# Performance work log

Hardware: AMD Instinct MI355X
Metric: run time of the kernel (lower is better)

## Reference

```python
import jax, jax.numpy as jnp
import numpy as np

B, L, D, RATIO = 256, 197, 768, 8
DK = D // RATIO  # 96


def _mk_linear(key, out_f, in_f):
    kw, kb = jax.random.split(key)
    W = jax.random.normal(kw, (out_f, in_f), jnp.float32) * 0.02  # xavier_normal gain=0.02 scale
    b = jax.random.normal(kb, (out_f,), jnp.float32) * 0.02
    return W, b


def setup_inputs() -> dict:
    key = jax.random.key(0)
    ks = jax.random.split(key, 10)
    x = jax.random.normal(ks[0], (B, L, D), jnp.float32)
    y = jax.random.normal(ks[1], (B, L, D), jnp.float32)
    Wk1, bk1 = _mk_linear(ks[2], DK, D)
    Wk2, bk2 = _mk_linear(ks[3], DK, D)
    Wks, bks = _mk_linear(ks[4], DK, DK)
    Wl1, bl1 = _mk_linear(ks[5], L, L)
    Wl2, bl2 = _mk_linear(ks[6], L, L)
    Wv1, bv1 = _mk_linear(ks[7], D, D)
    Wv2, bv2 = _mk_linear(ks[8], D, D)
    # torch inits gammas to 0; use small nonzero values so outputs/grads are non-trivial
    g = jax.random.normal(ks[9], (2,), jnp.float32) * 0.1
    gamma1 = g[:1]
    gamma2 = g[1:]
    return dict(x=x, y=y, Wk1=Wk1, bk1=bk1, Wk2=Wk2, bk2=bk2, Wks=Wks, bks=bks,
                Wl1=Wl1, bl1=bl1, Wl2=Wl2, bl2=bl2, Wv1=Wv1, bv1=bv1,
                Wv2=Wv2, bv2=bv2, gamma1=gamma1, gamma2=gamma2)


def reference(x, y, Wk1, bk1, Wk2, bk2, Wks, bks, Wl1, bl1, Wl2, bl2,
              Wv1, bv1, Wv2, bv2, gamma1, gamma2):
    b, l, d = x.shape
    # shared-projected keys (B, L, DK)
    k1 = (x @ Wk1.T + bk1) @ Wks.T + bks
    k2 = (y @ Wk2.T + bk2) @ Wks.T + bks
    # faithful to torch: .view(B, -1, L) is a raw reshape (scrambles layout), then permute
    k1r = k1.reshape(b, -1, l).swapaxes(1, 2)   # (B, L, DK)
    k2r = k2.reshape(b, -1, l)                  # (B, DK, L)
    energy = jnp.einsum('blc,bcm->blm', k1r, k2r)  # (B, L, L)
    att1 = jax.nn.softmax(energy @ Wl1.T + bl1, axis=-1)                   # att_y_on_x
    att2 = jax.nn.softmax(energy.swapaxes(1, 2) @ Wl2.T + bl2, axis=-1)    # att_x_on_y
    v2 = y @ Wv2.T + bv2  # (B, L, D)
    out_y_on_x = jnp.einsum('bdl,blm->bdm', v2.swapaxes(1, 2), att1).reshape(b, l, d)
    out_x = gamma1 * out_y_on_x + x
    v1 = x @ Wv1.T + bv1
    out_x_on_y = jnp.einsum('bdl,blm->bdm', v1.swapaxes(1, 2), att2).reshape(b, l, d)
    out_y = gamma2 * out_x_on_y + y
    return (out_x, out_y)
```

## Files before the change

### kernel.cpp

```cpp
#include <hip/hip_runtime.h>
#include <math.h>

typedef unsigned short ushort;
typedef __attribute__((ext_vector_type(8))) short short8;
typedef __attribute__((ext_vector_type(8))) unsigned short ushort8;
typedef __attribute__((ext_vector_type(4))) float f32x4;
typedef unsigned int u32;

#define VM_WAIT(N) asm volatile("s_waitcnt vmcnt(" #N ")" ::: "memory")
#define SBAR() asm volatile("s_barrier" ::: "memory")

__device__ __forceinline__ int swz4(int row) {
  return (row & 3) ^ ((row >> 2) & 3);
}

__device__ __forceinline__ ushort f2bf(float f) {
  u32 u = __float_as_uint(f);
  return (ushort)((u + 0x7FFF + ((u >> 16) & 1)) >> 16);
}
__device__ __forceinline__ float bf2f(ushort u) {
  u32 v = ((u32)u) << 16;
  return __uint_as_float(v);
}

__device__ __forceinline__ void gload16(const void* g, void* l) {
  __builtin_amdgcn_global_load_lds(
      (const __attribute__((address_space(1))) u32*)g,
      (__attribute__((address_space(3))) u32*)l, 16, 0, 0);
}

#define BKK 32
#define LDSP 68
__global__ __launch_bounds__(256) void gemm_generic(
    const float* __restrict__ A, const float* __restrict__ Bm, const float* __restrict__ Bm2,
    float* __restrict__ C, float* __restrict__ C2,
    int M, int N, int K, long sAi, long sAk, long sBj, long sBk, long sCi)
{
  __shared__ __align__(16) float lds_a[BKK * LDSP];
  __shared__ __align__(16) float lds_b[BKK * LDSP];
  const float* Bb = blockIdx.z ? Bm2 : Bm;
  float* Cc = blockIdx.z ? C2 : C;
  const int i0 = blockIdx.y * 64;
  const int j0 = blockIdx.x * 64;
  const int tid = threadIdx.x;
  const int tx = tid & 15, ty = tid >> 4;
  float acc[4][4] = {};
  for (int k0 = 0; k0 < K; k0 += BKK) {
    for (int idx = tid; idx < BKK * 64; idx += 256) {
      int kk = idx & (BKK - 1), ii = idx >> 5;
      int gi = i0 + ii, gk = k0 + kk;
      lds_a[kk * LDSP + ii] = (gi < M && gk < K) ? A[(long)gi * sAi + (long)gk * sAk] : 0.f;
    }
    for (int idx = tid; idx < BKK * 64; idx += 256) {
      int kk = idx & (BKK - 1), jj = idx >> 5;
      int gj = j0 + jj, gk = k0 + kk;
      lds_b[kk * LDSP + jj] = (gj < N && gk < K) ? Bb[(long)gj * sBj + (long)gk * sBk] : 0.f;
    }
    __syncthreads();
    #pragma unroll
    for (int kk = 0; kk < BKK; ++kk) {
      const float4 a4 = *reinterpret_cast<const float4*>(&lds_a[kk * LDSP + ty * 4]);
      const float4 b4 = *reinterpret_cast<const float4*>(&lds_b[kk * LDSP + tx * 4]);
      const float av[4] = {a4.x, a4.y, a4.z, a4.w};
      const float bv[4] = {b4.x, b4.y, b4.z, b4.w};
      #pragma unroll
      for (int a = 0; a < 4; ++a)
        #pragma unroll
        for (int b = 0; b < 4; ++b)
          acc[a][b] = fmaf(av[a], bv[b], acc[a][b]);
    }
    __syncthreads();
  }
  for (int a = 0; a < 4; ++a) {
    int gi = i0 + ty * 4 + a;
    if (gi >= M) continue;
    for (int b = 0; b < 4; ++b) {
      int gj = j0 + tx * 4 + b;
      if (gj >= N) continue;
      Cc[(long)gi * sCi + gj] = acc[a][b];
    }
  }
}

__global__ __launch_bounds__(256) void mfma_gemm(
    const ushort* __restrict__ A0, const ushort* __restrict__ A1,
    const ushort* __restrict__ B0, const ushort* __restrict__ B1,
    const float* __restrict__ bias0, const float* __restrict__ bias1,
    float* __restrict__ C0, float* __restrict__ C1,
    int M, int N, int K, long sAi, long sBj, long sCi)
{
  __shared__ ushort As[128 * 64];
  __shared__ ushort Bs[128 * 64];
  const int which = blockIdx.z;
  const ushort* Ab = which ? A1 : A0;
  const ushort* Bb = which ? B1 : B0;
  const float* bias = which ? bias1 : bias0;
  float* C = which ? C1 : C0;
  const int i0 = blockIdx.y * 128;
  const int j0 = blockIdx.x * 128;
  const int tid = threadIdx.x;
  const int wave = tid >> 6, lane = tid & 63;
  const int wm = wave >> 1, wn = wave & 1;
  const int col16 = lane & 15, krow = lane >> 4;

  f32x4 acc[4][4] = {};

  for (int k0 = 0; k0 < K; k0 += 64) {
    #pragma unroll
    for (int it = 0; it < 4; ++it) {
      int chunk = it * 256 + wave * 64 + lane;
      int row = chunk >> 3, s = chunk & 7;
      int kc = s ^ (row & 7);
      int gi = i0 + row; if (gi >= M) gi = M - 1;
      gload16(Ab + (long)gi * sAi + k0 + kc * 8, &As[chunk * 8]);
    }
    #pragma unroll
    for (int it = 0; it < 4; ++it) {
      int chunk = it * 256 + wave * 64 + lane;
      int row = chunk >> 3, s = chunk & 7;
      int kc = s ^ (row & 7);
      int gj = j0 + row; if (gj >= N) gj = N - 1;
      gload16(Bb + (long)gj * sBj + k0 + kc * 8, &Bs[chunk * 8]);
    }
    __syncthreads();
    #pragma unroll
    for (int ks = 0; ks < 2; ++ks) {
      short8 af[4], bfr[4];
      #pragma unroll
      for (int mi = 0; mi < 4; ++mi) {
        int row = wm * 64 + mi * 16 + col16;
        int slot = (ks * 4 + krow) ^ (row & 7);
        af[mi] = *(const short8*)&As[row * 64 + slot * 8];
      }
      #pragma unroll
      for (int nj = 0; nj < 4; ++nj) {
        int row = wn * 64 + nj * 16 + col16;
        int slot = (ks * 4 + krow) ^ (row & 7);
        bfr[nj] = *(const short8*)&Bs[row * 64 + slot * 8];
      }
      #pragma unroll
      for (int mi = 0; mi < 4; ++mi)
        #pragma unroll
        for (int nj = 0; nj < 4; ++nj)
          acc[mi][nj] = __builtin_amdgcn_mfma_f32_16x16x32_bf16(
              af[mi], bfr[nj], acc[mi][nj], 0, 0, 0);
    }
    __syncthreads();
  }

  const int r0 = krow * 4;
  #pragma unroll
  for (int mi = 0; mi < 4; ++mi) {
    int gi0 = i0 + wm * 64 + mi * 16 + r0;
    #pragma unroll
    for (int nj = 0; nj < 4; ++nj) {
      int gj = j0 + wn * 64 + nj * 16 + col16;
      f32x4 a = acc[mi][nj];
      #pragma unroll
      for (int r = 0; r < 4; ++r) {
        int gi = gi0 + r;
        if (gi >= M || gj >= N) continue;
        C[(long)gi * sCi + gj] = a[r] + bias[gj];
      }
    }
  }
}

__global__ __launch_bounds__(256) void att_gemm(
    const ushort* __restrict__ Wl0, const ushort* __restrict__ Wl1,
    const ushort* __restrict__ E0, const ushort* __restrict__ E1,
    const float* __restrict__ bl0, const float* __restrict__ bl1,
    ushort* __restrict__ a0, ushort* __restrict__ a1out)
{
  __shared__ ushort Aws[2][208 * 32];
  __shared__ ushort Bws[2][64 * 32];
  __shared__ float blds[208];
  const int which = blockIdx.z;
  const int bz = blockIdx.y;
  const ushort* Wl = which ? Wl1 : Wl0;
  const ushort* Bb = (which ? E1 : E0) + 50432L * bz;
  const float* bl = which ? bl1 : bl0;
  ushort* aout = which ? a1out : a0;
  const int l0 = blockIdx.x * 64;
  const int tid = threadIdx.x, wave = tid >> 6, lane = tid & 63;
  const int col16 = lane & 15, kq = lane >> 4;

  if (tid < 208) blds[tid] = (tid < 197) ? bl[tid] : 0.f;

  f32x4 acc[13] = {};

  auto stage = [&](int buf, int k0) {
    const int lrow = lane >> 2, s = lane & 3;
    #pragma unroll
    for (int c0 = 0; c0 < 5; ++c0) {
      int c = wave + c0 * 4;
      if (c >= 17) break;
      if (c < 13) {
        int row = c * 16 + lrow;
        int gr = row < 197 ? row : 196;
        int kc = s ^ swz4(row);
        gload16(Wl + (long)gr * 256 + k0 + kc * 8,
                (char*)(&Aws[buf][0]) + c * 1024 + lane * 16);
      } else {
        int row = (c - 13) * 16 + lrow;
        int gl = l0 + row; if (gl > 196) gl = 196;
        int kc = s ^ swz4(row);
        gload16(Bb + (long)gl * 256 + k0 + kc * 8,
                (char*)(&Bws[buf][0]) + (c - 13) * 1024 + lane * 16);
      }
    }
  };

  stage(0, 0);
  for (int t = 0; t < 7; ++t) {
    int cur = t & 1;
    if (t + 1 < 7) {
      stage(cur ^ 1, (t + 1) * 32);
      if (wave == 0) VM_WAIT(5); else VM_WAIT(4);
    } else {
      VM_WAIT(0);
    }
    SBAR();
    int brow = wave * 16 + col16;
    short8 bf = *(const short8*)((const char*)(&Bws[cur][0]) +
                                 brow * 64 + ((kq ^ swz4(brow)) << 4));
    #pragma unroll
    for (int j = 0; j < 13; ++j) {
      int arow = j * 16 + col16;
      short8 af = *(const short8*)((const char*)(&Aws[cur][0]) +
                                   arow * 64 + ((kq ^ swz4(arow)) << 4));
      acc[j] = __builtin_amdgcn_mfma_f32_16x16x32_bf16(af, bf, acc[j], 0, 0, 0);
    }
    SBAR();
  }

  const int c = l0 + wave * 16 + col16;
  float mx = -INFINITY;
  #pragma unroll
  for (int j = 0; j < 13; ++j)
    #pragma unroll
    for (int r = 0; r < 4; ++r) {
      int m = j * 16 + kq * 4 + r;
      float v = acc[j][r] + blds[m];
      v = (m < 197) ? v : -INFINITY;
      acc[j][r] = v;
      mx = fmaxf(mx, v);
    }
  mx = fmaxf(mx, __shfl_xor(mx, 16));
  mx = fmaxf(mx, __shfl_xor(mx, 32));
  float s = 0.f;
  #pragma unroll
  for (int j = 0; j < 13; ++j)
    #pragma unroll
    for (int r = 0; r < 4; ++r) {
      int m = j * 16 + kq * 4 + r;
      float e = (m < 197) ? __expf(acc[j][r] - mx) : 0.f;
      acc[j][r] = e;
      s += e;
    }
  s += __shfl_xor(s, 16);
  s += __shfl_xor(s, 32);
  const float inv = 1.f / s;
  ushort* ab = aout + 50432L * bz;
  #pragma unroll
  for (int j = 0; j < 13; ++j)
    #pragma unroll
    for (int r = 0; r < 4; ++r) {
      int m = j * 16 + kq * 4 + r;
      if (m < 197)
        ab[(long)m * 256 + c] = (c < 197) ? f2bf(acc[j][r] * inv) : (ushort)0;
    }
}

__global__ __launch_bounds__(256) void vout_gemm(
    const ushort* __restrict__ A0, const ushort* __restrict__ A1,
    const ushort* __restrict__ B0, const ushort* __restrict__ B1,
    const float* __restrict__ bias0, const float* __restrict__ bias1,
    const ushort* __restrict__ resid0, const ushort* __restrict__ resid1,
    const float* __restrict__ g0, const float* __restrict__ g1,
    void* __restrict__ C0, void* __restrict__ C1,
    int N, int K, long sAi, long bAs, long sBj, long bBs,
    long sCi, long bCs, int mtiles, int batches, int mode)
{
  __shared__ ushort As[2][128 * 32];
  __shared__ ushort Bs[2][224 * 32];
  const int per = mtiles * batches;
  int bid = blockIdx.x;
  const int which = bid / per;
  bid -= which * per;
  const ushort* A = which ? A1 : A0;
  const ushort* Bm = which ? B1 : B0;
  const float* bias = which ? bias1 : bias0;
  const ushort* resid = which ? resid1 : resid0;
  const float* gammaPtr = which ? g1 : g0;
  void* C = which ? C1 : C0;

  int mtile, bz;
  if ((batches & 7) == 0) {
    int xcd = bid & 7, sid = bid >> 3;
    mtile = sid % mtiles;
    bz = (sid / mtiles) * 8 + xcd;
  } else {
    mtile = bid % mtiles;
    bz = bid / mtiles;
  }
  const ushort* Ab = A + bAs * bz + (long)(mtile * 128) * sAi;
  const ushort* Bb = Bm + bBs * bz;
  const int tid = threadIdx.x, wave = tid >> 6, lane = tid & 63;
  const int wr = wave >> 1, wc = wave & 1;
  const int col16 = lane & 15, kq = lane >> 4;

  f32x4 acc[4][7] = {};

  auto stage = [&](int buf, int k0) {
    const int lrow = lane >> 2, s = lane & 3;
    #pragma unroll
    for (int c0 = 0; c0 < 6; ++c0) {
      int c = wave + c0 * 4;
      if (c >= 22) break;
      if (c < 8) {
        int row = c * 16 + lrow;
        int kc = s ^ swz4(row);
        gload16(Ab + (long)row * sAi + k0 + kc * 8,
                (char*)(&As[buf][0]) + c * 1024 + lane * 16);
      } else {
        int row = (c - 8) * 16 + lrow;
        int gj = row < N ? row : N - 1;
        int kc = s ^ swz4(row);
        gload16(Bb + (long)gj * sBj + k0 + kc * 8,
                (char*)(&Bs[buf][0]) + (c - 8) * 1024 + lane * 16);
      }
    }
  };

  const int nt = K >> 5;
  stage(0, 0);
  for (int t = 0; t < nt; ++t) {
    int cur = t & 1;
    if (t + 1 < nt) {
      stage(cur ^ 1, (t + 1) << 5);
      if (wave < 2) VM_WAIT(6); else VM_WAIT(5);
    } else {
      VM_WAIT(0);
    }
    SBAR();
    short8 af[4];
    #pragma unroll
    for (int mi = 0; mi < 4; ++mi) {
      int arow = wr * 64 + mi * 16 + col16;
      af[mi] = *(const short8*)((const char*)(&As[cur][0]) +
                                arow * 64 + ((kq ^ swz4(arow)) << 4));
    }
    #pragma unroll
    for (int nj = 0; nj < 7; ++nj) {
      int brow = wc * 112 + nj * 16 + col16;
      short8 bf = *(const short8*)((const char*)(&Bs[cur][0]) +
                                   brow * 64 + ((kq ^ swz4(brow)) << 4));
      #pragma unroll
      for (int mi = 0; mi < 4; ++mi)
        acc[mi][nj] = __builtin_amdgcn_mfma_f32_16x16x32_bf16(
            af[mi], bf, acc[mi][nj], 0, 0, 0);
    }
    SBAR();
  }

  if (mode == 3) {
    const float g = gammaPtr[0];
    #pragma unroll
    for (int mi = 0; mi < 4; ++mi)
      #pragma unroll
      for (int nj = 0; nj < 7; ++nj) {
        int gj = wc * 112 + nj * 16 + col16;
        if (gj >= N) continue;
        #pragma unroll
        for (int r = 0; r < 4; ++r) {
          int gi = mtile * 128 + wr * 64 + mi * 16 + kq * 4 + r;
          long ci = bCs * bz + (long)gi * sCi + gj;
          ((float*)C)[ci] = g * acc[mi][nj][r] + bf2f(resid[ci]);
        }
      }
  } else {
    #pragma unroll
    for (int mi = 0; mi < 4; ++mi)
      #pragma unroll
      for (int r = 0; r < 4; ++r) {
        int gi = mtile * 128 + wr * 64 + mi * 16 + kq * 4 + r;
        long base = bCs * bz + (long)gi * sCi;
        #pragma unroll
        for (int nj = 0; nj < 7; ++nj) {
          int gj = wc * 112 + nj * 16 + col16;
          ((ushort*)C)[base + gj] = (gj < N) ? f2bf(acc[mi][nj][r] + bias[gi])
                                             : (ushort)0;
        }
      }
  }
}

__global__ __launch_bounds__(256) void energy_dual(
    const float* __restrict__ k1, const float* __restrict__ k2,
    ushort* __restrict__ Eb, ushort* __restrict__ ETb)
{
  __shared__ __align__(16) float lds[2][BKK * LDSP];
  const int bz = blockIdx.z;
  const float* Ab = k1 + 18912L * bz;
  const float* Bb = k2 + 18912L * bz;
  const int i0 = blockIdx.y * 64;
  const int j0 = blockIdx.x * 64;
  const int tid = threadIdx.x;
  const int tx = tid & 15, ty = tid >> 4;
  float acc[4][4] = {};
  for (int k0 = 0; k0 < 96; k0 += BKK) {
    for (int idx = tid; idx < BKK * 64; idx += 256) {
      int ii = idx & 63, kk = idx >> 6;
      int gi = i0 + ii, gk = k0 + kk;
      lds[0][kk * LDSP + ii] = (gi < 197 && gk < 96) ? Ab[(long)gk * 197 + gi] : 0.f;
    }
    for (int idx = tid; idx < BKK * 64; idx += 256) {
      int jj = idx & 63, kk = idx >> 6;
      int gj = j0 + jj, gk = k0 + kk;
      lds[1][kk * LDSP + jj] = (gj < 197 && gk < 96) ? Bb[(long)gk * 197 + gj] : 0.f;
    }
    __syncthreads();
    #pragma unroll
    for (int kk = 0; kk < BKK; ++kk) {
      const float4 a4 = *reinterpret_cast<const float4*>(&lds[0][kk * LDSP + ty * 4]);
      const float4 b4 = *reinterpret_cast<const float4*>(&lds[1][kk * LDSP + tx * 4]);
      const float av[4] = {a4.x, a4.y, a4.z, a4.w};
      const float bv[4] = {b4.x, b4.y, b4.z, b4.w};
      #pragma unroll
      for (int a = 0; a < 4; ++a)
        #pragma unroll
        for (int b = 0; b < 4; ++b)
          acc[a][b] = fmaf(av[a], bv[b], acc[a][b]);
    }
    __syncthreads();
  }
  float* trans = &lds[0][0];
  #pragma unroll
  for (int a = 0; a < 4; ++a)
    #pragma unroll
    for (int b = 0; b < 4; ++b)
      trans[(ty * 4 + a) * 68 + tx * 4 + b] = acc[a][b];
  __syncthreads();
  #pragma unroll
  for (int a2 = 0; a2 < 4; ++a2) {
    int lrow = ty * 4 + a2;
    int gl = i0 + lrow;
    if (gl < 197) {
      #pragma unroll
      for (int b2 = 0; b2 < 4; ++b2) {
        int gm = j0 + tx + 16 * b2;
        float v = trans[lrow * 68 + tx + 16 * b2];
        Eb[bz * 50432L + (long)gl * 256 + gm] = (gm < 197) ? f2bf(v) : (ushort)0;
      }
    }
  }
  #pragma unroll
  for (int a2 = 0; a2 < 4; ++a2) {
    int mrow = ty * 4 + a2;
    int gm = j0 + mrow;
    if (gm < 197) {
      #pragma unroll
      for (int b2 = 0; b2 < 4; ++b2) {
        int gl = i0 + tx + 16 * b2;
        float v = trans[(tx + 16 * b2) * 68 + mrow];
        ETb[bz * 50432L + (long)gm * 256 + gl] = (gl < 197) ? f2bf(v) : (ushort)0;
      }
    }
  }
}

__global__ void fuse_bias2(const float* __restrict__ Wks,
                           const float* __restrict__ bk1, const float* __restrict__ bk2,
                           const float* __restrict__ bks,
                           float* __restrict__ bf1, float* __restrict__ bf2) {
  int c = threadIdx.x;
  if (c >= 192) return;
  const float* bk = (c < 96) ? bk1 : bk2;
  float* bf = (c < 96) ? bf1 : bf2;
  int cc = (c < 96) ? c : c - 96;
  float s = bks[cc];
  for (int e = 0; e < 96; ++e) s += Wks[cc * 96 + e] * bk[e];
  bf[cc] = s;
}

__global__ __launch_bounds__(256) void conv_weights(
    const float* __restrict__ Wf1, const float* __restrict__ Wf2,
    const float* __restrict__ Wv1, const float* __restrict__ Wv2,
    const float* __restrict__ Wl1, const float* __restrict__ Wl2,
    ushort* __restrict__ Wf1b, ushort* __restrict__ Wf2b,
    ushort* __restrict__ Wv1b, ushort* __restrict__ Wv2b,
    ushort* __restrict__ Wl1b, ushort* __restrict__ Wl2b)
{
  const long total = 147456 + 1179648 + 100864;
  long stride = (long)gridDim.x * blockDim.x;
  for (long i = (long)blockIdx.x * blockDim.x + threadIdx.x; i < total; i += stride) {
    if (i < 147456) {
      long j = i;
      if (j < 73728) Wf1b[j] = f2bf(Wf1[j]);
      else Wf2b[j - 73728] = f2bf(Wf2[j - 73728]);
    } else if (i < 147456 + 1179648) {
      long j = i - 147456;
      if (j < 589824) Wv1b[j] = f2bf(Wv1[j]);
      else Wv2b[j - 589824] = f2bf(Wv2[j - 589824]);
    } else {
      long j = i - 147456 - 1179648;
      int w2 = j >= 50432;
      if (w2) j -= 50432;
      int r = (int)(j >> 8), cc = (int)(j & 255);
      const float* s = w2 ? Wl2 : Wl1;
      ushort* d = w2 ? Wl2b : Wl1b;
      d[j] = (cc < 197) ? f2bf(s[(long)r * 197 + cc]) : (ushort)0;
    }
  }
}

__global__ __launch_bounds__(256) void conv_xy(const float* __restrict__ x,
                                               const float* __restrict__ y,
                                               ushort* __restrict__ xb,
                                               ushort* __restrict__ yb, long n8) {
  long i = (long)blockIdx.x * blockDim.x + threadIdx.x;
  long stride = (long)gridDim.x * blockDim.x;
  for (; i < 2 * n8; i += stride) {
    const float* s = (i < n8) ? x : y;
    ushort* d = (i < n8) ? xb : yb;
    long j = (i < n8) ? i : i - n8;
    float4 a = ((const float4*)s)[2 * j];
    float4 b = ((const float4*)s)[2 * j + 1];
    ushort8 o;
    o[0] = f2bf(a.x); o[1] = f2bf(a.y); o[2] = f2bf(a.z); o[3] = f2bf(a.w);
    o[4] = f2bf(b.x); o[5] = f2bf(b.y); o[6] = f2bf(b.z); o[7] = f2bf(b.w);
    *(ushort8*)&d[j * 8] = o;
  }
}

extern "C" void kernel_launch(void* const* d_in, const int* in_sizes, int n_in,
                              void* d_out, int out_size, void* d_ws, size_t ws_size,
                              hipStream_t stream) {
  const float* x   = (const float*)d_in[0];
  const float* y   = (const float*)d_in[1];
  const float* Wk1 = (const float*)d_in[2];
  const float* bk1 = (const float*)d_in[3];
  const float* Wk2 = (const float*)d_in[4];
  const float* bk2 = (const float*)d_in[5];
  const float* Wks = (const float*)d_in[6];
  const float* bks = (const float*)d_in[7];
  const float* Wl1 = (const float*)d_in[8];
  const float* bl1 = (const float*)d_in[9];
  const float* Wl2 = (const float*)d_in[10];
  const float* bl2 = (const float*)d_in[11];
  const float* Wv1 = (const float*)d_in[12];
  const float* bv1 = (const float*)d_in[13];
  const float* Wv2 = (const float*)d_in[14];
  const float* bv2 = (const float*)d_in[15];
  const float* gamma1 = (const float*)d_in[16];
  const float* gamma2 = (const float*)d_in[17];
  float* out = (float*)d_out;

  const int B = 256, L = 197, D = 768;
  const long LD  = (long)L * D;
  const long LDK = (long)L * 96;

  const size_t staticBytes = 3446784;
  const size_t perB = 605184 + 151296 + 201728 + 201728 + 786432;
  int Bc = 256;
  while (Bc > 8 && staticBytes + (size_t)Bc * perB > ws_size) Bc >>= 1;

  char* p = (char*)d_ws;
  auto carve = [&](size_t bytes) { char* r = p; p += bytes; return r; };
  float*  Wf1   = (float*)carve(73728 * 4);
  float*  Wf2   = (float*)carve(73728 * 4);
  float*  bf1   = (float*)carve(512);
  float*  bf2   = (float*)carve(512);
  ushort* Wv1b  = (ushort*)carve(589824 * 2);
  ushort* Wv2b  = (ushort*)carve(589824 * 2);
  ushort* Wf1b  = (ushort*)carve(73728 * 2);
  ushort* Wf2b  = (ushort*)carve(73728 * 2);
  ushort* Wl1b  = (ushort*)carve(50432 * 2);
  ushort* Wl2b  = (ushort*)carve(50432 * 2);
  ushort* xb    = (ushort*)carve((size_t)Bc * LD * 2);
  ushort* yb    = (ushort*)carve((size_t)Bc * LD * 2);
  float*  k1    = (float*)carve((size_t)Bc * LDK * 4);
  float*  k2    = (float*)carve((size_t)Bc * LDK * 4);
  ushort* Eb    = (ushort*)carve((size_t)Bc * 50432 * 2);
  ushort* ETbuf = (ushort*)carve((size_t)Bc * 50432 * 2);
  ushort* a1    = (ushort*)carve((size_t)Bc * 50432 * 2);
  ushort* a2    = (ushort*)carve((size_t)Bc * 50432 * 2);
  ushort* vT    = (ushort*)carve((size_t)Bc * 196608 * 2);
  ushort* vT2   = (ushort*)carve((size_t)Bc * 196608 * 2);

  dim3 blk(256);

  gemm_generic<<<dim3(12, 2, 2), blk, 0, stream>>>(Wks, Wk1, Wk2, Wf1, Wf2,
      96, 768, 96, 96, 1, 1, 768, 768);
  fuse_bias2<<<1, 192, 0, stream>>>(Wks, bk1, bk2, bks, bf1, bf2);
  conv_weights<<<dim3(1024), blk, 0, stream>>>(Wf1, Wf2, Wv1, Wv2, Wl1, Wl2,
      Wf1b, Wf2b, Wv1b, Wv2b, Wl1b, Wl2b);

  for (int c0 = 0; c0 < B; c0 += Bc) {
    const float* xc = x + (long)c0 * LD;
    const float* yc = y + (long)c0 * LD;
    const int Mr = Bc * L;
    const int gym = (Mr + 127) / 128;

    conv_xy<<<dim3(2048), blk, 0, stream>>>(xc, yc, xb, yb, (long)Bc * LD / 8);

    mfma_gemm<<<dim3(1, gym, 2), blk, 0, stream>>>(xb, yb, Wf1b, Wf2b, bf1, bf2,
        k1, k2, Mr, 96, 768, 768, 768, 96);

    energy_dual<<<dim3(4, 4, Bc), blk, 0, stream>>>(k1, k2, Eb, ETbuf);

    att_gemm<<<dim3(4, Bc, 2), blk, 0, stream>>>(Wl1b, Wl2b, Eb, ETbuf,
        bl1, bl2, a1, a2);

    vout_gemm<<<dim3(12 * Bc), blk, 0, stream>>>(Wv2b, Wv1b, yb, xb, bv2, bv1,
        nullptr, nullptr, nullptr, nullptr, vT, vT2,
        197, 768, 768, 0, 768, LD, 256, 196608, 6, Bc, 1);

    vout_gemm<<<dim3(12 * Bc), blk, 0, stream>>>(vT, vT2, a1, a2, nullptr, nullptr,
        xb, yb, gamma1, gamma2,
        out + (long)c0 * LD, out + (long)B * LD + (long)c0 * LD,
        197, 224, 256, 196608, 256, 50432, 197, LD, 6, Bc, 3);
  }
}
```

Baseline: 752.1 us.

## Replace per-batch V projection GEMM with one large batched-N GEMM

The value projection (Wv @ x^T) moves out of the per-batch vout_gemm path into a new vbig_gemm kernel. It treats all batches as one wide N dimension, padded to 224 columns per batch, and uses 128x128 tiles. This drops the wasted padded 224-column B tile per batch and reuses weight tiles across batches, and it shrinks the vT workspace from 256 to 224 columns per batch. The output GEMM now reads vT with the new stride, and the mode branch is removed. The risk is weaker L2 locality for the weight matrix and the cost of the extra index math done per load.

```diff
diff --git a/kernel.cpp b/kernel.cpp
--- a/kernel.cpp
+++ b/kernel.cpp
@@ -166,6 +166,105 @@
   }
 }
 
+__global__ __launch_bounds__(256) void vbig_gemm(
+    const ushort* __restrict__ A0, const ushort* __restrict__ A1,
+    const ushort* __restrict__ B0, const ushort* __restrict__ B1,
+    const float* __restrict__ bias0, const float* __restrict__ bias1,
+    ushort* __restrict__ C0, ushort* __restrict__ C1,
+    int ntiles, long Nc)
+{
+  __shared__ ushort As[2][128 * 32];
+  __shared__ ushort Bs[2][128 * 32];
+  const int per = 6 * ntiles;
+  int bid = blockIdx.x;
+  const int which = bid / per;
+  bid -= which * per;
+  const int ntile = bid % ntiles;
+  const int mtile = bid / ntiles;
+  const ushort* Ab = (which ? A1 : A0) + (long)(mtile * 128) * 768;
+  const ushort* Bb = which ? B1 : B0;
+  const float* bias = which ? bias1 : bias0;
+  ushort* C = which ? C1 : C0;
+  const int n0 = ntile * 128;
+  const int tid = threadIdx.x, wave = tid >> 6, lane = tid & 63;
+  const int wm = wave >> 1, wn = wave & 1;
+  const int col16 = lane & 15, kq = lane >> 4;
+
+  f32x4 acc[4][4] = {};
+
+  auto stage = [&](int buf, int k0) {
+    const int lrow = lane >> 2, s = lane & 3;
+    #pragma unroll
+    for (int c0 = 0; c0 < 4; ++c0) {
+      int c = wave * 4 + c0;
+      if (c < 8) {
+        int row = c * 16 + lrow;
+        int kc = s ^ swz4(row);
+        gload16(Ab + (long)row * 768 + k0 + kc * 8,
+                (char*)(&As[buf][0]) + c * 1024 + lane * 16);
+      } else {
+        int j = (c - 8) * 16 + lrow;
+        int n = n0 + j;
+        int b = n / 224;
+        int l = n - b * 224;
+        int grow = b * 197 + (l < 197 ? l : 196);
+        int kc = s ^ swz4(j);
+        gload16(Bb + (long)grow * 768 + k0 + kc * 8,
+                (char*)(&Bs[buf][0]) + (c - 8) * 1024 + lane * 16);
+      }
+    }
+  };
+
+  stage(0, 0);
+  for (int t = 0; t < 24; ++t) {
+    int cur = t & 1;
+    if (t + 1 < 24) {
+      stage(cur ^ 1, (t + 1) << 5);
+      VM_WAIT(4);
+    } else {
+      VM_WAIT(0);
+    }
+    SBAR();
+    short8 af[4], bfr[4];
+    #pragma unroll
+    for (int mi = 0; mi < 4; ++mi) {
+      int arow = wm * 64 + mi * 16 + col16;
+      af[mi] = *(const short8*)((const char*)(&As[cur][0]) +
+                                arow * 64 + ((kq ^ swz4(arow)) << 4));
+    }
+    #pragma unroll
+    for (int nj = 0; nj < 4; ++nj) {
+      int brow = wn * 64 + nj * 16 + col16;
+      bfr[nj] = *(const short8*)((const char*)(&Bs[cur][0]) +
+                                 brow * 64 + ((kq ^ swz4(brow)) << 4));
+    }
+    #pragma unroll
+    for (int mi = 0; mi < 4; ++mi)
+      #pragma unroll
+      for (int nj = 0; nj < 4; ++nj)
+        acc[mi][nj] = __builtin_amdgcn_mfma_f32_16x16x32_bf16(
+            af[mi], bfr[nj], acc[mi][nj], 0, 0, 0);
+    SBAR();
+  }
+
+  #pragma unroll
+  for (int mi = 0; mi < 4; ++mi) {
+    #pragma unroll
+    for (int r = 0; r < 4; ++r) {
+      int gi = mtile * 128 + wm * 64 + mi * 16 + kq * 4 + r;
+      float bv = bias[gi];
+      long base = (long)gi * Nc;
+      #pragma unroll
+      for (int nj = 0; nj < 4; ++nj) {
+        int n = n0 + wn * 64 + nj * 16 + col16;
+        int b = n / 224;
+        int l = n - b * 224;
+        C[base + n] = (l < 197) ? f2bf(acc[mi][nj][r] + bv) : (ushort)0;
+      }
+    }
+  }
+}
+
 __global__ __launch_bounds__(256) void att_gemm(
     const ushort* __restrict__ Wl0, const ushort* __restrict__ Wl1,
     const ushort* __restrict__ E0, const ushort* __restrict__ E1,
@@ -275,12 +374,11 @@
 __global__ __launch_bounds__(256) void vout_gemm(
     const ushort* __restrict__ A0, const ushort* __restrict__ A1,
     const ushort* __restrict__ B0, const ushort* __restrict__ B1,
-    const float* __restrict__ bias0, const float* __restrict__ bias1,
     const ushort* __restrict__ resid0, const ushort* __restrict__ resid1,
     const float* __restrict__ g0, const float* __restrict__ g1,
-    void* __restrict__ C0, void* __restrict__ C1,
+    float* __restrict__ C0, float* __restrict__ C1,
     int N, int K, long sAi, long bAs, long sBj, long bBs,
-    long sCi, long bCs, int mtiles, int batches, int mode)
+    long sCi, long bCs, int mtiles, int batches)
 {
   __shared__ ushort As[2][128 * 32];
   __shared__ ushort Bs[2][224 * 32];
@@ -290,10 +388,9 @@
   bid -= which * per;
   const ushort* A = which ? A1 : A0;
   const ushort* Bm = which ? B1 : B0;
-  const float* bias = which ? bias1 : bias0;
   const ushort* resid = which ? resid1 : resid0;
   const float* gammaPtr = which ? g1 : g0;
-  void* C = which ? C1 : C0;
+  float* C = which ? C1 : C0;
 
   int mtile, bz;
   if ((batches & 7) == 0) {
@@ -364,36 +461,20 @@
     SBAR();
   }
 
-  if (mode == 3) {
-    const float g = gammaPtr[0];
-    #pragma unroll
-    for (int mi = 0; mi < 4; ++mi)
-      #pragma unroll
-      for (int nj = 0; nj < 7; ++nj) {
-        int gj = wc * 112 + nj * 16 + col16;
-        if (gj >= N) continue;
-        #pragma unroll
-        for (int r = 0; r < 4; ++r) {
-          int gi = mtile * 128 + wr * 64 + mi * 16 + kq * 4 + r;
-          long ci = bCs * bz + (long)gi * sCi + gj;
-          ((float*)C)[ci] = g * acc[mi][nj][r] + bf2f(resid[ci]);
-        }
-      }
-  } else {
-    #pragma unroll
-    for (int mi = 0; mi < 4; ++mi)
+  const float g = gammaPtr[0];
+  #pragma unroll
+  for (int mi = 0; mi < 4; ++mi)
+    #pragma unroll
+    for (int nj = 0; nj < 7; ++nj) {
+      int gj = wc * 112 + nj * 16 + col16;
+      if (gj >= N) continue;
       #pragma unroll
       for (int r = 0; r < 4; ++r) {
         int gi = mtile * 128 + wr * 64 + mi * 16 + kq * 4 + r;
-        long base = bCs * bz + (long)gi * sCi;
-        #pragma unroll
-        for (int nj = 0; nj < 7; ++nj) {
-          int gj = wc * 112 + nj * 16 + col16;
-          ((ushort*)C)[base + gj] = (gj < N) ? f2bf(acc[mi][nj][r] + bias[gi])
-                                             : (ushort)0;
-        }
-      }
-  }
+        long ci = bCs * bz + (long)gi * sCi + gj;
+        C[ci] = g * acc[mi][nj][r] + bf2f(resid[ci]);
+      }
+    }
 }
 
 __global__ __launch_bounds__(256) void energy_dual(
@@ -562,7 +643,7 @@
   const long LDK = (long)L * 96;
 
   const size_t staticBytes = 3446784;
-  const size_t perB = 605184 + 151296 + 201728 + 201728 + 786432;
+  const size_t perB = 605184 + 151296 + 201728 + 201728 + 688128;
   int Bc = 256;
   while (Bc > 8 && staticBytes + (size_t)Bc * perB > ws_size) Bc >>= 1;
 
@@ -586,8 +667,9 @@
   ushort* ETbuf = (ushort*)carve((size_t)Bc * 50432 * 2);
   ushort* a1    = (ushort*)carve((size_t)Bc * 50432 * 2);
   ushort* a2    = (ushort*)carve((size_t)Bc * 50432 * 2);
-  ushort* vT    = (ushort*)carve((size_t)Bc * 196608 * 2);
-  ushort* vT2   = (ushort*)carve((size_t)Bc * 196608 * 2);
+  const long Nc = (long)Bc * 224;
+  ushort* vT    = (ushort*)carve((size_t)768 * Nc * 2);
+  ushort* vT2   = (ushort*)carve((size_t)768 * Nc * 2);
 
   dim3 blk(256);
 
@@ -613,13 +695,15 @@
     att_gemm<<<dim3(4, Bc, 2), blk, 0, stream>>>(Wl1b, Wl2b, Eb, ETbuf,
         bl1, bl2, a1, a2);
 
-    vout_gemm<<<dim3(12 * Bc), blk, 0, stream>>>(Wv2b, Wv1b, yb, xb, bv2, bv1,
-        nullptr, nullptr, nullptr, nullptr, vT, vT2,
-        197, 768, 768, 0, 768, LD, 256, 196608, 6, Bc, 1);
-
-    vout_gemm<<<dim3(12 * Bc), blk, 0, stream>>>(vT, vT2, a1, a2, nullptr, nullptr,
+    {
+      int ntiles = (int)(Nc / 128);
+      vbig_gemm<<<dim3(2 * 6 * ntiles), blk, 0, stream>>>(
+          Wv2b, Wv1b, yb, xb, bv2, bv1, vT, vT2, ntiles, Nc);
+    }
+
+    vout_gemm<<<dim3(12 * Bc), blk, 0, stream>>>(vT, vT2, a1, a2,
         xb, yb, gamma1, gamma2,
         out + (long)c0 * LD, out + (long)B * LD + (long)c0 * LD,
-        197, 224, 256, 196608, 256, 50432, 197, LD, 6, Bc, 3);
-  }
-}
+        197, 224, Nc, 224, 256, 50432, 197, LD, 6, Bc);
+  }
+}
```

New measurement: 703.8 us. 6.4% less time.
